# Kernel tuning notes

Measured on AMD Instinct MI355X. Metric: run time of the kernel, lower is better.

The kernel has to match this reference:

```python
import jax, jax.numpy as jnp
import numpy as np

P = 100   # num_proxies
N = 1024  # num_samples
D = 512


def _edge_index():
    # complete bipartite proxy<->sample graph, both directions, plus self-loops
    # (PyG GATConv adds self-loops for all nodes by default)
    p = np.arange(P)
    s = np.arange(P, P + N)
    src_ps = np.repeat(p, N)   # proxy -> sample
    dst_ps = np.tile(s, P)
    loops = np.arange(P + N)
    src = np.concatenate([src_ps, dst_ps, loops]).astype(np.int32)
    dst = np.concatenate([dst_ps, src_ps, loops]).astype(np.int32)
    return jnp.asarray(src), jnp.asarray(dst)


def setup_inputs() -> dict:
    key = jax.random.key(0)
    ks = jax.random.split(key, 10)
    sc = 1.0 / np.sqrt(D)
    src, dst = _edge_index()
    return {
        "x": jax.random.normal(ks[0], (N, D), jnp.float32),
        "proxies": jax.random.normal(ks[1], (P, D), jnp.float32),
        "W1": jax.random.normal(ks[2], (D, D), jnp.float32) * sc,
        "a_src1": jax.random.normal(ks[3], (D,), jnp.float32) * sc,
        "a_dst1": jax.random.normal(ks[4], (D,), jnp.float32) * sc,
        "b1": jnp.zeros((D,), jnp.float32),
        "W2": jax.random.normal(ks[5], (D, D), jnp.float32) * sc,
        "a_src2": jax.random.normal(ks[6], (D,), jnp.float32) * sc,
        "a_dst2": jax.random.normal(ks[7], (D,), jnp.float32) * sc,
        "b2": jnp.zeros((D,), jnp.float32),
        "fc_w": jax.random.normal(ks[8], (D, 100), jnp.float32) * sc,
        "fc_b": jnp.zeros((100,), jnp.float32),
        "src": src,
        "dst": dst,
    }


def _gat_conv(x, src, dst, W, a_src, a_dst, b, n_nodes):
    # PyG GATConv, heads=1, concat=True, negative_slope=0.2
    h = x @ W                      # [n, D]
    l_src = h @ a_src              # [n]
    l_dst = h @ a_dst              # [n]
    e = jax.nn.leaky_relu(l_src[src] + l_dst[dst], 0.2)   # [E]
    # segment softmax over edges sharing the same destination
    e = e - jax.ops.segment_max(e, dst, num_segments=n_nodes)[dst]
    ex = jnp.exp(e)
    denom = jax.ops.segment_sum(ex, dst, num_segments=n_nodes)[dst]
    alpha = ex / denom             # [E]
    out = jax.ops.segment_sum(alpha[:, None] * h[src], dst, num_segments=n_nodes)
    return out + b


def reference(x, proxies, W1, a_src1, a_dst1, b1, W2, a_src2, a_dst2, b2, fc_w, fc_b, src, dst):
    n = P + N
    h = jnp.concatenate([proxies, x], axis=0)          # [P+N, D]
    h = jax.nn.relu(_gat_conv(h, src, dst, W1, a_src1, a_dst1, b1, n))
    # Dropout -> identity (eval)
    h = jax.nn.relu(_gat_conv(h, src, dst, W2, a_src2, a_dst2, b2, n))
    preds = h @ fc_w + fc_b                            # [P+N, 100]
    return preds[P:], h[P:]
```

## Files before the change

### kernel.cpp

```cpp
#include <hip/hip_runtime.h>

#define PP 100
#define NS 1024
#define NN 1124
#define DD 512
#define CC 100
#define NTHR 256
#define GT  512

typedef _Float16 f16;
typedef _Float16 f16x8 __attribute__((ext_vector_type(8)));
typedef float    f32x4 __attribute__((ext_vector_type(4)));

__device__ __forceinline__ float lk(float v) { return v > 0.f ? v : 0.2f * v; }
__device__ __forceinline__ f16 hif(float v) { return (f16)v; }
__device__ __forceinline__ f16 lof(float v) { return (f16)(v - (float)((f16)v)); }

#define MFMA16(a, b, c) __builtin_amdgcn_mfma_f32_16x16x32_f16(a, b, c, 0, 0, 0)


__device__ __forceinline__ void mgemm_core(
    const f16* __restrict__ Ah, const f16* __restrict__ Al,
    const f16* __restrict__ Bth, const f16* __restrict__ Btl,
    int K, int row0, int col0, f16* __restrict__ lds, f32x4 acc[2])
{
  const int t = threadIdx.x;
  const int lane = t & 63, w = t >> 6;
  const int wr = w >> 1, wc = w & 1;
  const bool isA = t < 256;
  const int tt = t & 255;
  const int srow = tt >> 2, su = tt & 3;
  const int lw = srow * 40 + su * 8;
  const int sec0 = isA ? 0 : 5120, sec1 = isA ? 2560 : 7680;
  const f16* g0 = isA ? Ah : Bth;
  const f16* g1 = isA ? Al : Btl;
  const size_t goff = (size_t)((isA ? row0 : col0) + srow) * K + su * 8;
  const int fra = wr * 16 + (lane & 15);
  const int frb = wc * 32 + (lane & 15);
  const int fu  = (lane >> 4) * 8;
  f32x4 p0 = *(const f32x4*)(g0 + goff);
  f32x4 p1 = *(const f32x4*)(g1 + goff);
  *(f32x4*)(lds + sec0 + lw) = p0;
  *(f32x4*)(lds + sec1 + lw) = p1;
  if (K > 32) {
    p0 = *(const f32x4*)(g0 + goff + 32);
    p1 = *(const f32x4*)(g1 + goff + 32);
  }
  __syncthreads();
  int cur = 0;
  for (int kt = 32; kt <= K; kt += 32) {
    f16* rb = lds + cur * 10240;
    f16* wb = lds + (cur ^ 1) * 10240;
    f16x8 ah  = *(const f16x8*)(rb + fra * 40 + fu);
    f16x8 al  = *(const f16x8*)(rb + 2560 + fra * 40 + fu);
    f16x8 bh0 = *(const f16x8*)(rb + 5120 + frb * 40 + fu);
    f16x8 bl0 = *(const f16x8*)(rb + 7680 + frb * 40 + fu);
    f16x8 bh1 = *(const f16x8*)(rb + 5120 + (frb + 16) * 40 + fu);
    f16x8 bl1 = *(const f16x8*)(rb + 7680 + (frb + 16) * 40 + fu);
    if (kt < K) {
      *(f32x4*)(wb + sec0 + lw) = p0;
      *(f32x4*)(wb + sec1 + lw) = p1;
      if (kt + 32 < K) {
        p0 = *(const f32x4*)(g0 + goff + kt + 32);
        p1 = *(const f32x4*)(g1 + goff + kt + 32);
      }
    }
    acc[0] = MFMA16(ah, bh0, acc[0]);
    acc[0] = MFMA16(al, bh0, acc[0]);
    acc[0] = MFMA16(ah, bl0, acc[0]);
    acc[1] = MFMA16(ah, bh1, acc[1]);
    acc[1] = MFMA16(al, bh1, acc[1]);
    acc[1] = MFMA16(ah, bl1, acc[1]);
    __syncthreads();
    cur ^= 1;
  }
}

__device__ __forceinline__ void agg_core(
    const float* __restrict__ lsrc, int kvalid,
    const float* __restrict__ ldb, const float* __restrict__ lsb,
    const f16* __restrict__ Bth, const f16* __restrict__ Btl,
    int K, int row0, int col0, int rvalid,
    const float* __restrict__ selfv,
    f16* __restrict__ outh, f16* __restrict__ outl,
    f16* __restrict__ lds, float* __restrict__ fred)
{
  const int t = threadIdx.x, lane = t & 63, w = t >> 6;
  const int wr = w >> 1, wc = w & 1;
  float* zred = fred;
  float* res  = fred + 256;
  float* riz  = fred + 320;
  float sm = -1e30f;
  for (int k = t; k < kvalid; k += GT) sm = fmaxf(sm, lsrc[k]);
#pragma unroll
  for (int off = 1; off < 64; off <<= 1) sm = fmaxf(sm, __shfl_xor(sm, off));
  if (lane == 0) zred[w] = sm;
  __syncthreads();
  sm = fmaxf(fmaxf(fmaxf(zred[0], zred[1]), fmaxf(zred[2], zred[3])),
             fmaxf(fmaxf(zred[4], zred[5]), fmaxf(zred[6], zred[7])));
  __syncthreads();
  const bool isA = t < 256;
  const int tt = t & 255;
  const int srow = tt >> 2, su = tt & 3;
  const int lw = srow * 40 + su * 8;
  bool rok = false; float ldr = 0.f, mr = 0.f;
  if (isA && (row0 + srow) < rvalid) {
    rok = true;
    ldr = ldb[row0 + srow];
    mr  = lk(fmaxf(sm, lsb[row0 + srow]) + ldr);
  }
  const size_t boff = (size_t)(col0 + srow) * K + su * 8;
  const int fra = wr * 16 + (lane & 15);
  const int frb = wc * 32 + (lane & 15);
  const int fu  = (lane >> 4) * 8;
  f32x4 acc[2] = {};
  float zacc = 0.f;
  f32x4 p0, p1;
  if (isA) {
    p0 = *(const f32x4*)(lsrc + su * 8);
    p1 = *(const f32x4*)(lsrc + su * 8 + 4);
  } else {
    p0 = *(const f32x4*)(Bth + boff);
    p1 = *(const f32x4*)(Btl + boff);
  }
  auto stage = [&](f16* buf, int kbase) {
    if (isA) {
      f16x8 ae, al8;
#pragma unroll
      for (int j = 0; j < 8; ++j) {
        const int k = kbase + su * 8 + j;
        const float lv = (j < 4) ? p0[j] : p1[j - 4];
        float f = 0.f;
        if (rok && k < kvalid) f = __expf(lk(lv + ldr) - mr);
        zacc += f;
        ae[j] = hif(f); al8[j] = lof(f);
      }
      *(f16x8*)(buf + lw) = ae;
      *(f16x8*)(buf + 2560 + lw) = al8;
    } else {
      *(f32x4*)(buf + 5120 + lw) = p0;
      *(f32x4*)(buf + 7680 + lw) = p1;
    }
  };
  auto prefetch = [&](int k) {
    if (isA) {
      p0 = *(const f32x4*)(lsrc + k + su * 8);
      p1 = *(const f32x4*)(lsrc + k + su * 8 + 4);
    } else {
      p0 = *(const f32x4*)(Bth + boff + k);
      p1 = *(const f32x4*)(Btl + boff + k);
    }
  };
  stage(lds, 0);
  if (K > 32) prefetch(32);
  __syncthreads();
  int cur = 0;
  for (int kt = 32; kt <= K; kt += 32) {
    f16* rb = lds + cur * 10240;
    f16* wb = lds + (cur ^ 1) * 10240;
    f16x8 ah  = *(const f16x8*)(rb + fra * 40 + fu);
    f16x8 al  = *(const f16x8*)(rb + 2560 + fra * 40 + fu);
    f16x8 bh0 = *(const f16x8*)(rb + 5120 + frb * 40 + fu);
    f16x8 bl0 = *(const f16x8*)(rb + 7680 + frb * 40 + fu);
    f16x8 bh1 = *(const f16x8*)(rb + 5120 + (frb + 16) * 40 + fu);
    f16x8 bl1 = *(const f16x8*)(rb + 7680 + (frb + 16) * 40 + fu);
    if (kt < K) {
      stage(wb, kt);
      if (kt + 32 < K) prefetch(kt + 32);
    }
    acc[0] = MFMA16(ah, bh0, acc[0]);
    acc[0] = MFMA16(al, bh0, acc[0]);
    acc[0] = MFMA16(ah, bl0, acc[0]);
    acc[1] = MFMA16(ah, bh1, acc[1]);
    acc[1] = MFMA16(al, bh1, acc[1]);
    acc[1] = MFMA16(ah, bl1, acc[1]);
    __syncthreads();
    cur ^= 1;
  }
  if (t < 256) zred[t] = zacc;
  __syncthreads();
  if (t < 64) {
    float z = zred[t * 4] + zred[t * 4 + 1] + zred[t * 4 + 2] + zred[t * 4 + 3];
    float es = 0.f, iz = 0.f;
    if (row0 + t < rvalid) {
      const float l2 = ldb[row0 + t], s2 = lsb[row0 + t];
      const float m2 = lk(fmaxf(sm, s2) + l2);
      es = __expf(lk(s2 + l2) - m2);
      iz = 1.f / (z + es);
    }
    res[t] = es; riz[t] = iz;
  }
  __syncthreads();
#pragma unroll
  for (int q = 0; q < 4; ++q) {
    const int rl = wr * 16 + (lane >> 4) * 4 + q;
    const int gr = row0 + rl;
    if (gr >= rvalid) continue;
    const float es = res[rl], iz = riz[rl];
#pragma unroll
    for (int n = 0; n < 2; ++n) {
      const int c = col0 + wc * 32 + n * 16 + (lane & 15);
      const float v = (acc[n][q] + es * selfv[(size_t)gr * DD + c]) * iz;
      outh[(size_t)gr * DD + c] = hif(v);
      outl[(size_t)gr * DD + c] = lof(v);
    }
  }
}

__device__ __forceinline__ void cvt_tile(
    const float* __restrict__ in, int R, int Cin,
    f16* __restrict__ oh, f16* __restrict__ ol, int ldo,
    int ti, int tj)
{
  const int t = threadIdx.x;
  const int gj0 = tj * 64 + (t & 31) * 2;
  const int i8  = (t >> 5) * 8;
  const bool c0 = gj0 < Cin, c1 = (gj0 + 1) < Cin;
  f16x8 vh0, vl0, vh1, vl1;
#pragma unroll
  for (int e = 0; e < 8; ++e) {
    const int gi = ti * 64 + i8 + e;
    float a = 0.f, b = 0.f;
    if (gi < R) {
      if (c0 && c1) {
        const float2 v = *(const float2*)(in + (size_t)gi * Cin + gj0);
        a = v.x; b = v.y;
      } else if (c0) {
        a = in[(size_t)gi * Cin + gj0];
      }
    }
    vh0[e] = hif(a); vl0[e] = lof(a);
    vh1[e] = hif(b); vl1[e] = lof(b);
  }
  const size_t o0 = (size_t)gj0 * ldo + ti * 64 + i8;
  *(f16x8*)(oh + o0) = vh0;
  *(f16x8*)(ol + o0) = vl0;
  const size_t o1 = o0 + ldo;
  *(f16x8*)(oh + o1) = vh1;
  *(f16x8*)(ol + o1) = vl1;
}

__global__ __launch_bounds__(NTHR) void prep1_k(
    const float* __restrict__ W1, const float* __restrict__ W2,
    const float* __restrict__ as1, const float* __restrict__ ad1,
    const float* __restrict__ as2, const float* __restrict__ ad2,
    float* __restrict__ v1s, float* __restrict__ v1d,
    float* __restrict__ v2s, float* __restrict__ v2d,
    float* __restrict__ ls2, float* __restrict__ ld2,
    float* __restrict__ M1pf, float* __restrict__ zP)
{
  const int u = blockIdx.x;
  if (u < 256) {
    const int wid  = u * 4 + (threadIdx.x >> 6);
    const int lane = threadIdx.x & 63;
    const int r = wid & 511;
    const bool l1 = (wid < 512);
    const float* W = l1 ? W1 : W2;
    const float4* a4 = (const float4*)(l1 ? as1 : as2);
    const float4* b4 = (const float4*)(l1 ? ad1 : ad2);
    const float4* w4 = (const float4*)(W + (size_t)r * DD);
    float4 w0 = w4[lane], w1 = w4[lane + 64];
    float4 a0 = a4[lane], a1 = a4[lane + 64];
    float4 b0 = b4[lane], b1 = b4[lane + 64];
    float s1 = w0.x * a0.x + w0.y * a0.y + w0.z * a0.z + w0.w * a0.w
             + w1.x * a1.x + w1.y * a1.y + w1.z * a1.z + w1.w * a1.w;
    float s2 = w0.x * b0.x + w0.y * b0.y + w0.z * b0.z + w0.w * b0.w
             + w1.x * b1.x + w1.y * b1.y + w1.z * b1.z + w1.w * b1.w;
#pragma unroll
    for (int off = 32; off > 0; off >>= 1) {
      s1 += __shfl_down(s1, off);
      s2 += __shfl_down(s2, off);
    }
    if (lane == 0) {
      (l1 ? v1s : v2s)[r] = s1;
      (l1 ? v1d : v2d)[r] = s2;
    }
  } else if (u == 256) {
    for (int i = threadIdx.x; i < 1152; i += NTHR) { ls2[i] = 0.f; ld2[i] = 0.f; }
    if (threadIdx.x < 128) zP[threadIdx.x] = 0.f;
  } else {
    float4* p4 = (float4*)M1pf + (size_t)(u - 257) * 800;
#pragma unroll
    for (int p = 0; p < 4; ++p) {
      const int i = threadIdx.x + p * 256;
      if (i < 800) p4[i] = make_float4(0.f, 0.f, 0.f, 0.f);
    }
  }
}

__global__ __launch_bounds__(NTHR) void prep2_k(
    const float* __restrict__ x, const float* __restrict__ prox,
    const float* __restrict__ W1, const float* __restrict__ W2,
    const float* __restrict__ fcw,
    const float* __restrict__ v1s, const float* __restrict__ v1d,
    f16* xth, f16* xtl, f16* pth, f16* ptl,
    f16* W1th, f16* W1tl, f16* W2th, f16* W2tl, f16* fwth, f16* fwtl,
    float* __restrict__ ls1, float* __restrict__ ld1)
{
  const int b = blockIdx.x;
  if (b < 64) {
    cvt_tile(W1, 512, 512, W1th, W1tl, 512, b >> 3, b & 7);
  } else if (b < 128) {
    cvt_tile(W2, 512, 512, W2th, W2tl, 512, (b - 64) >> 3, (b - 64) & 7);
  } else if (b < 256) {
    cvt_tile(x, NS, 512, xth, xtl, NS, (b - 128) >> 3, (b - 128) & 7);
  } else if (b < 272) {
    cvt_tile(prox, PP, 512, pth, ptl, 128, (b - 256) >> 3, (b - 256) & 7);
  } else if (b < 288) {
    cvt_tile(fcw, 512, CC, fwth, fwtl, 512, (b - 272) >> 1, (b - 272) & 1);
  } else {
    const int r    = (b - 288) * 4 + (threadIdx.x >> 6);
    const int lane = threadIdx.x & 63;
    if (r >= NN) return;
    const float* row = (r < PP) ? prox + (size_t)r * DD
                                : x + (size_t)(r - PP) * DD;
    const float4* r4 = (const float4*)row;
    const float4* s4 = (const float4*)v1s;
    const float4* d4 = (const float4*)v1d;
    float4 v0 = r4[lane], v1 = r4[lane + 64];
    float4 a0 = s4[lane], a1 = s4[lane + 64];
    float4 b0 = d4[lane], b1 = d4[lane + 64];
    float s1 = v0.x * a0.x + v0.y * a0.y + v0.z * a0.z + v0.w * a0.w
             + v1.x * a1.x + v1.y * a1.y + v1.z * a1.z + v1.w * a1.w;
    float s2 = v0.x * b0.x + v0.y * b0.y + v0.z * b0.z + v0.w * b0.w
             + v1.x * b1.x + v1.y * b1.y + v1.z * b1.z + v1.w * b1.w;
#pragma unroll
    for (int off = 32; off > 0; off >>= 1) {
      s1 += __shfl_down(s1, off);
      s2 += __shfl_down(s2, off);
    }
    if (lane == 0) { ls1[r] = s1; ld1[r] = s2; }
  }
}

__global__ __launch_bounds__(GT) void agg1x_k(
    const float* __restrict__ ls1, const float* __restrict__ ld1,
    const f16* __restrict__ pth, const f16* __restrict__ ptl,
    const f16* __restrict__ xth, const f16* __restrict__ xtl,
    const float* __restrict__ x,
    float* __restrict__ M1pf, float* __restrict__ zP,
    f16* __restrict__ M1h, f16* __restrict__ M1l)
{
  __shared__ __align__(16) f16 lds[20480];
  __shared__ float fred[384];
  const int b = blockIdx.x;
  if (b < 128) {
    const int row0 = (b >> 3) * 64, col0 = (b & 7) * 64;
    agg_core(ls1, PP, ld1 + PP, ls1 + PP, pth, ptl, 128, row0, col0, NS,
             x, M1h + (size_t)PP * DD, M1l + (size_t)PP * DD, lds, fred);
    return;
  }
  const int t = threadIdx.x, lane = t & 63, w = t >> 6;
  const int wr = w >> 1, wc = w & 1;
  const int b2 = b - 128;
  const int tile = b2 >> 2, chunk = b2 & 3;
  const int row0 = (tile >> 3) * 64, col0 = (tile & 7) * 64;
  const int k0 = chunk * 256;
  const float* lsrc = ls1 + PP;
  float sm = -1e30f;
  for (int k = t; k < NS; k += GT) sm = fmaxf(sm, lsrc[k]);
#pragma unroll
  for (int off = 1; off < 64; off <<= 1) sm = fmaxf(sm, __shfl_xor(sm, off));
  if (lane == 0) fred[w] = sm;
  __syncthreads();
  sm = fmaxf(fmaxf(fmaxf(fred[0], fred[1]), fmaxf(fred[2], fred[3])),
             fmaxf(fmaxf(fred[4], fred[5]), fmaxf(fred[6], fred[7])));
  __syncthreads();
  const bool isA = t < 256;
  const int tt = t & 255;
  const int srow = tt >> 2, su = tt & 3;
  const int lw = srow * 40 + su * 8;
  bool rok = false; float ldr = 0.f, mr = 0.f;
  if (isA && (row0 + srow) < PP) {
    rok = true;
    ldr = ld1[row0 + srow];
    mr  = lk(fmaxf(sm, ls1[row0 + srow]) + ldr);
  }
  const size_t boff = (size_t)(col0 + srow) * NS + k0 + su * 8;
  const int fra = wr * 16 + (lane & 15);
  const int frb = wc * 32 + (lane & 15);
  const int fu  = (lane >> 4) * 8;
  f32x4 acc[2] = {};
  float zacc = 0.f;
  f32x4 p0, p1;
  auto prefetch = [&](int k) {
    if (isA) {
      p0 = *(const f32x4*)(lsrc + k0 + k + su * 8);
      p1 = *(const f32x4*)(lsrc + k0 + k + su * 8 + 4);
    } else {
      p0 = *(const f32x4*)(xth + boff + k);
      p1 = *(const f32x4*)(xtl + boff + k);
    }
  };
  auto stage = [&](f16* buf) {
    if (isA) {
      f16x8 ae, al8;
#pragma unroll
      for (int j = 0; j < 8; ++j) {
        const float lv = (j < 4) ? p0[j] : p1[j - 4];
        float f = 0.f;
        if (rok) f = __expf(lk(lv + ldr) - mr);
        zacc += f;
        ae[j] = hif(f); al8[j] = lof(f);
      }
      *(f16x8*)(buf + lw) = ae;
      *(f16x8*)(buf + 2560 + lw) = al8;
    } else {
      *(f32x4*)(buf + 5120 + lw) = p0;
      *(f32x4*)(buf + 7680 + lw) = p1;
    }
  };
  prefetch(0);
  stage(lds);
  prefetch(32);
  __syncthreads();
  int cur = 0;
  for (int kt = 32; kt <= 256; kt += 32) {
    f16* rb = lds + cur * 10240;
    f16* wb = lds + (cur ^ 1) * 10240;
    f16x8 ah  = *(const f16x8*)(rb + fra * 40 + fu);
    f16x8 al  = *(const f16x8*)(rb + 2560 + fra * 40 + fu);
    f16x8 bh0 = *(const f16x8*)(rb + 5120 + frb * 40 + fu);
    f16x8 bl0 = *(const f16x8*)(rb + 7680 + frb * 40 + fu);
    f16x8 bh1 = *(const f16x8*)(rb + 5120 + (frb + 16) * 40 + fu);
    f16x8 bl1 = *(const f16x8*)(rb + 7680 + (frb + 16) * 40 + fu);
    if (kt < 256) {
      stage(wb);
      if (kt + 32 < 256) prefetch(kt + 32);
    }
    acc[0] = MFMA16(ah, bh0, acc[0]);
    acc[0] = MFMA16(al, bh0, acc[0]);
    acc[0] = MFMA16(ah, bl0, acc[0]);
    acc[1] = MFMA16(ah, bh1, acc[1]);
    acc[1] = MFMA16(al, bh1, acc[1]);
    acc[1] = MFMA16(ah, bl1, acc[1]);
    __syncthreads();
    cur ^= 1;
  }
  if (col0 == 0) {
    if (t < 256) fred[t] = zacc;
    __syncthreads();
    if (t < 64) {
      const int r = row0 + t;
      if (r < PP) {
        float z = fred[t * 4] + fred[t * 4 + 1] + fred[t * 4 + 2] + fred[t * 4 + 3];
        atomicAdd(&zP[r], z);
      }
    }
  }
#pragma unroll
  for (int q = 0; q < 4; ++q) {
    const int gr = row0 + wr * 16 + (lane >> 4) * 4 + q;
    if (gr >= PP) continue;
#pragma unroll
    for (int n = 0; n < 2; ++n) {
      const int c = col0 + wc * 32 + n * 16 + (lane & 15);
      atomicAdd(&M1pf[(size_t)gr * DD + c], acc[n][q]);
    }
  }
}

__global__ __launch_bounds__(GT) void h1_k(
    const f16* __restrict__ M1h, const f16* __restrict__ M1l,
    const float* __restrict__ M1pf, const float* __restrict__ zP,
    const float* __restrict__ ls1, const float* __restrict__ ld1,
    const float* __restrict__ prox,
    const f16* __restrict__ W1th, const f16* __restrict__ W1tl,
    const float* __restrict__ b1,
    const float* __restrict__ v2s, const float* __restrict__ v2d,
    float* __restrict__ h1, f16* __restrict__ h1pth, f16* __restrict__ h1ptl,
    float* __restrict__ ls2, float* __restrict__ ld2)
{
  __shared__ __align__(16) f16 lds[20480];
  __shared__ float fred[384];
  float* esA = fred + 256;
  float* izA = fred + 320;
  const int t = threadIdx.x, lane = t & 63, w = t >> 6;
  const int wr = w >> 1, wc = w & 1;
  const int b = blockIdx.x;
  const int row0 = (b >> 3) * 64, col0 = (b & 7) * 64;
  const bool hasP = (row0 < 128);
  if (hasP) {
    float sm = -1e30f;
    for (int k = t; k < NS; k += GT) sm = fmaxf(sm, ls1[PP + k]);
#pragma unroll
    for (int off = 1; off < 64; off <<= 1) sm = fmaxf(sm, __shfl_xor(sm, off));
    if (lane == 0) fred[w] = sm;
    __syncthreads();
    sm = fmaxf(fmaxf(fmaxf(fred[0], fred[1]), fmaxf(fred[2], fred[3])),
               fmaxf(fmaxf(fred[4], fred[5]), fmaxf(fred[6], fred[7])));
    if (t < 64) {
      const int r = row0 + t;
      float es = 0.f, iz = 0.f;
      if (r < PP) {
        const float ldr = ld1[r];
        const float m = lk(fmaxf(sm, ls1[r]) + ldr);
        es = __expf(lk(ls1[r] + ldr) - m);
        iz = 1.f / (zP[r] + es);
      }
      esA[t] = es; izA[t] = iz;
    }
    __syncthreads();
  }
  const bool isA = t < 256;
  const int tt = t & 255;
  const int srow = tt >> 2, su = tt & 3;
  const int lw = srow * 40 + su * 8;
  const int ar = row0 + srow;
  const bool isP = isA && (ar < PP);
  const size_t aoff = (size_t)ar * DD + su * 8;
  const size_t boff = (size_t)(col0 + srow) * DD + su * 8;
  const int fra = wr * 16 + (lane & 15);
  const int frb = wc * 32 + (lane & 15);
  const int fu  = (lane >> 4) * 8;
  const float esr = isP ? esA[srow] : 0.f;
  const float izr = isP ? izA[srow] : 0.f;
  f32x4 qa0, qa1, qb0, qb1;
  auto loadS = [&](int k) {
    if (isA) {
      if (isP) {
        qa0 = *(const f32x4*)(M1pf + aoff + k);
        qa1 = *(const f32x4*)(M1pf + aoff + k + 4);
        qb0 = *(const f32x4*)(prox + aoff + k);
        qb1 = *(const f32x4*)(prox + aoff + k + 4);
      } else {
        qa0 = *(const f32x4*)(M1h + aoff + k);
        qa1 = *(const f32x4*)(M1l + aoff + k);
      }
    } else {
      qa0 = *(const f32x4*)(W1th + boff + k);
      qa1 = *(const f32x4*)(W1tl + boff + k);
    }
  };
  auto storeS = [&](f16* wb) {
    if (isA) {
      if (isP) {
        f16x8 hh, ll;
#pragma unroll
        for (int j = 0; j < 8; ++j) {
          const float pv = (j < 4) ? qa0[j] : qa1[j - 4];
          const float xv = (j < 4) ? qb0[j] : qb1[j - 4];
          const float v = (pv + esr * xv) * izr;
          hh[j] = hif(v); ll[j] = lof(v);
        }
        *(f16x8*)(wb + lw) = hh;
        *(f16x8*)(wb + 2560 + lw) = ll;
      } else {
        *(f32x4*)(wb + lw) = qa0;
        *(f32x4*)(wb + 2560 + lw) = qa1;
      }
    } else {
      *(f32x4*)(wb + 5120 + lw) = qa0;
      *(f32x4*)(wb + 7680 + lw) = qa1;
    }
  };
  f32x4 acc[2] = {};
  loadS(0);
  storeS(lds);
  loadS(32);
  __syncthreads();
  int cur = 0;
  for (int kt = 32; kt <= DD; kt += 32) {
    f16* rb = lds + cur * 10240;
    f16* wb = lds + (cur ^ 1) * 10240;
    f16x8 ah  = *(const f16x8*)(rb + fra * 40 + fu);
    f16x8 al  = *(const f16x8*)(rb + 2560 + fra * 40 + fu);
    f16x8 bh0 = *(const f16x8*)(rb + 5120 + frb * 40 + fu);
    f16x8 bl0 = *(const f16x8*)(rb + 7680 + frb * 40 + fu);
    f16x8 bh1 = *(const f16x8*)(rb + 5120 + (frb + 16) * 40 + fu);
    f16x8 bl1 = *(const f16x8*)(rb + 7680 + (frb + 16) * 40 + fu);
    if (kt < DD) {
      storeS(wb);
      if (kt + 32 < DD) loadS(kt + 32);
    }
    acc[0] = MFMA16(ah, bh0, acc[0]);
    acc[0] = MFMA16(al, bh0, acc[0]);
    acc[0] = MFMA16(ah, bl0, acc[0]);
    acc[1] = MFMA16(ah, bh1, acc[1]);
    acc[1] = MFMA16(al, bh1, acc[1]);
    acc[1] = MFMA16(ah, bl1, acc[1]);
    __syncthreads();
    cur ^= 1;
  }
  const int c0 = col0 + wc * 32 + (lane & 15);
  const int c1 = c0 + 16;
  const float vs0 = v2s[c0], vs1 = v2s[c1];
  const float vd0 = v2d[c0], vd1 = v2d[c1];
  const float bb0 = b1[c0],  bb1 = b1[c1];
#pragma unroll
  for (int q = 0; q < 4; ++q) {
    const int r = row0 + wr * 16 + (lane >> 4) * 4 + q;
    if (r >= NN) continue;
    float ps = 0.f, pd = 0.f;
#pragma unroll
    for (int n = 0; n < 2; ++n) {
      const int c = (n == 0) ? c0 : c1;
      const float v = fmaxf(acc[n][q] + (n == 0 ? bb0 : bb1), 0.f);
      h1[(size_t)r * DD + c] = v;
      ps += v * (n == 0 ? vs0 : vs1);
      pd += v * (n == 0 ? vd0 : vd1);
      if (r < 128) {
        const size_t o = (size_t)c * 128 + r;
        f16 hh = (f16)0.f, ll = (f16)0.f;
        if (r < PP) { hh = hif(v); ll = lof(v); }
        h1pth[o] = hh; h1ptl[o] = ll;
      }
    }
#pragma unroll
    for (int off = 1; off < 16; off <<= 1) {
      ps += __shfl_xor(ps, off);
      pd += __shfl_xor(pd, off);
    }
    if ((lane & 15) == 0) {
      atomicAdd(&ls2[r], ps);
      atomicAdd(&ld2[r], pd);
    }
  }
}

__global__ __launch_bounds__(GT) void agg2x_k(
    const float* __restrict__ ls2, const float* __restrict__ ld2,
    const f16* __restrict__ h1pth, const f16* __restrict__ h1ptl,
    const float* __restrict__ h1,
    f16* __restrict__ M2h, f16* __restrict__ M2l)
{
  __shared__ __align__(16) f16 lds[20480];
  __shared__ float fred[384];
  const int b = blockIdx.x;
  const int row0 = (b >> 3) * 64, col0 = (b & 7) * 64;
  agg_core(ls2, PP, ld2 + PP, ls2 + PP, h1pth, h1ptl, 128, row0, col0, NS,
           h1 + (size_t)PP * DD, M2h, M2l, lds, fred);
}

__global__ __launch_bounds__(GT) void h2_k(
    const f16* __restrict__ M2h, const f16* __restrict__ M2l,
    const f16* __restrict__ W2th, const f16* __restrict__ W2tl,
    const float* __restrict__ b2, float* __restrict__ h2s,
    f16* __restrict__ h2h, f16* __restrict__ h2l)
{
  __shared__ __align__(16) f16 lds[20480];
  f32x4 acc[2] = {};
  const int t = threadIdx.x, lane = t & 63, w = t >> 6;
  const int wr = w >> 1, wc = w & 1;
  const int b = blockIdx.x;
  const int row0 = (b >> 3) * 64, col0 = (b & 7) * 64;
  mgemm_core(M2h, M2l, W2th, W2tl, DD, row0, col0, lds, acc);
#pragma unroll
  for (int q = 0; q < 4; ++q) {
    const int r = row0 + wr * 16 + (lane >> 4) * 4 + q;
#pragma unroll
    for (int n = 0; n < 2; ++n) {
      const int c = col0 + wc * 32 + n * 16 + (lane & 15);
      const float v = fmaxf(acc[n][q] + b2[c], 0.f);
      const size_t o = (size_t)r * DD + c;
      h2s[o] = v;
      h2h[o] = hif(v); h2l[o] = lof(v);
    }
  }
}

__global__ __launch_bounds__(GT) void fc_k(
    const f16* __restrict__ h2h, const f16* __restrict__ h2l,
    const f16* __restrict__ fwth, const f16* __restrict__ fwtl,
    const float* __restrict__ fcb, float* __restrict__ out)
{
  __shared__ __align__(16) f16 lds[20480];
  f32x4 acc[2] = {};
  const int t = threadIdx.x, lane = t & 63, w = t >> 6;
  const int wr = w >> 1, wc = w & 1;
  const int b = blockIdx.x;
  const int row0 = (b >> 1) * 64, col0 = (b & 1) * 64;
  mgemm_core(h2h, h2l, fwth, fwtl, DD, row0, col0, lds, acc);
#pragma unroll
  for (int q = 0; q < 4; ++q) {
    const int r = row0 + wr * 16 + (lane >> 4) * 4 + q;
#pragma unroll
    for (int n = 0; n < 2; ++n) {
      const int c = col0 + wc * 32 + n * 16 + (lane & 15);
      if (c < CC) out[(size_t)r * CC + c] = acc[n][q] + fcb[c];
    }
  }
}

extern "C" void kernel_launch(void* const* d_in, const int* in_sizes, int n_in,
                              void* d_out, int out_size, void* d_ws, size_t ws_size,
                              hipStream_t stream)
{
  const float* x    = (const float*)d_in[0];
  const float* prox = (const float*)d_in[1];
  const float* W1   = (const float*)d_in[2];
  const float* as1  = (const float*)d_in[3];
  const float* ad1  = (const float*)d_in[4];
  const float* b1   = (const float*)d_in[5];
  const float* W2   = (const float*)d_in[6];
  const float* as2  = (const float*)d_in[7];
  const float* ad2  = (const float*)d_in[8];
  const float* b2   = (const float*)d_in[9];
  const float* fcw  = (const float*)d_in[10];
  const float* fcb  = (const float*)d_in[11];
  float* out = (float*)d_out;

  float* F = (float*)d_ws;
  float* h1   = F; F += (size_t)NN * DD;
  float* ls1  = F; F += 1152;
  float* ld1  = F; F += 1152;
  float* ls2  = F; F += 1152;
  float* ld2  = F; F += 1152;
  float* v1s  = F; F += DD;
  float* v1d  = F; F += DD;
  float* v2s  = F; F += DD;
  float* v2d  = F; F += DD;
  float* M1pf = F; F += (size_t)128 * DD;
  float* zP   = F; F += 128;
  f16* H = (f16*)F;
  f16* M1h  = H; H += (size_t)1152 * DD;
  f16* M1l  = H; H += (size_t)1152 * DD;
  f16* M2h  = H; H += (size_t)NS * DD;
  f16* M2l  = H; H += (size_t)NS * DD;
  f16* xth  = H; H += (size_t)DD * NS;
  f16* xtl  = H; H += (size_t)DD * NS;
  f16* pth  = H; H += (size_t)DD * 128;
  f16* ptl  = H; H += (size_t)DD * 128;
  f16* W1th = H; H += (size_t)DD * DD;
  f16* W1tl = H; H += (size_t)DD * DD;
  f16* W2th = H; H += (size_t)DD * DD;
  f16* W2tl = H; H += (size_t)DD * DD;
  f16* fwth = H; H += (size_t)128 * DD;
  f16* fwtl = H; H += (size_t)128 * DD;
  f16* h2h  = H; H += (size_t)NS * DD;
  f16* h2l  = H; H += (size_t)NS * DD;
  f16* h1pth = H; H += (size_t)DD * 128;
  f16* h1ptl = H; H += (size_t)DD * 128;
  float* h2s = out + (size_t)NS * CC;

  prep1_k<<<dim3(273), dim3(NTHR), 0, stream>>>(W1, W2, as1, ad1, as2, ad2,
                                                v1s, v1d, v2s, v2d, ls2, ld2,
                                                M1pf, zP);
  prep2_k<<<dim3(569), dim3(NTHR), 0, stream>>>(x, prox, W1, W2, fcw, v1s, v1d,
      xth, xtl, pth, ptl, W1th, W1tl, W2th, W2tl, fwth, fwtl, ls1, ld1);
  agg1x_k<<<dim3(192), dim3(GT), 0, stream>>>(ls1, ld1, pth, ptl, xth, xtl,
                                              x, M1pf, zP, M1h, M1l);
  h1_k<<<dim3(144), dim3(GT), 0, stream>>>(M1h, M1l, M1pf, zP, ls1, ld1, prox,
                                           W1th, W1tl, b1, v2s, v2d,
                                           h1, h1pth, h1ptl, ls2, ld2);
  agg2x_k<<<dim3(128), dim3(GT), 0, stream>>>(ls2, ld2, h1pth, h1ptl, h1,
                                              M2h, M2l);
  h2_k<<<dim3(128), dim3(GT), 0, stream>>>(M2h, M2l, W2th, W2tl, b2,
                                           h2s, h2h, h2l);
  fc_k<<<dim3(32), dim3(GT), 0, stream>>>(h2h, h2l, fwth, fwtl, fcb, out);
}
```

Baseline: 140.3 us.

## Widen GEMM K-tile to 128 and split h2 to f16 pairs inside fc kernel

All MFMA GEMM loops now stage 128-wide K tiles per double-buffer step instead of 32, with a padded row stride and more registers for prefetch. This cuts the number of loop iterations and barriers and gives each global load more bytes. LDS per block grows to about 136KB, which limits occupancy to one block per CU. Separately, h2_k no longer writes f16 hi/lo copies of h2; fc_k reads the fp32 h2 and splits it while staging, removing one intermediate round trip through global memory.

```diff
diff --git a/kernel.cpp b/kernel.cpp
--- a/kernel.cpp
+++ b/kernel.cpp
@@ -18,6 +18,11 @@
 
 #define MFMA16(a, b, c) __builtin_amdgcn_mfma_f32_16x16x32_f16(a, b, c, 0, 0, 0)
 
+#define LROW   136
+#define SEC_AL 8704
+#define SEC_BH 17408
+#define SEC_BL 26112
+#define BUFSZ  34816
 
 __device__ __forceinline__ void mgemm_core(
     const f16* __restrict__ Ah, const f16* __restrict__ Al,
@@ -30,47 +35,62 @@
   const bool isA = t < 256;
   const int tt = t & 255;
   const int srow = tt >> 2, su = tt & 3;
-  const int lw = srow * 40 + su * 8;
-  const int sec0 = isA ? 0 : 5120, sec1 = isA ? 2560 : 7680;
+  const int lw = srow * LROW + su * 32;
+  const int sec0 = isA ? 0 : SEC_BH, sec1 = isA ? SEC_AL : SEC_BL;
   const f16* g0 = isA ? Ah : Bth;
   const f16* g1 = isA ? Al : Btl;
-  const size_t goff = (size_t)((isA ? row0 : col0) + srow) * K + su * 8;
+  const size_t goff = (size_t)((isA ? row0 : col0) + srow) * K + su * 32;
   const int fra = wr * 16 + (lane & 15);
   const int frb = wc * 32 + (lane & 15);
   const int fu  = (lane >> 4) * 8;
-  f32x4 p0 = *(const f32x4*)(g0 + goff);
-  f32x4 p1 = *(const f32x4*)(g1 + goff);
-  *(f32x4*)(lds + sec0 + lw) = p0;
-  *(f32x4*)(lds + sec1 + lw) = p1;
-  if (K > 32) {
-    p0 = *(const f32x4*)(g0 + goff + 32);
-    p1 = *(const f32x4*)(g1 + goff + 32);
-  }
+  f32x4 p[8];
+  auto pf = [&](int k) {
+#pragma unroll
+    for (int i = 0; i < 4; ++i) {
+      p[i]     = *(const f32x4*)(g0 + goff + k + i * 8);
+      p[4 + i] = *(const f32x4*)(g1 + goff + k + i * 8);
+    }
+  };
+  auto st = [&](f16* buf) {
+#pragma unroll
+    for (int i = 0; i < 4; ++i) {
+      *(f32x4*)(buf + sec0 + lw + i * 8) = p[i];
+      *(f32x4*)(buf + sec1 + lw + i * 8) = p[4 + i];
+    }
+  };
+  pf(0); st(lds);
+  if (K > 128) pf(128);
   __syncthreads();
   int cur = 0;
-  for (int kt = 32; kt <= K; kt += 32) {
-    f16* rb = lds + cur * 10240;
-    f16* wb = lds + (cur ^ 1) * 10240;
-    f16x8 ah  = *(const f16x8*)(rb + fra * 40 + fu);
-    f16x8 al  = *(const f16x8*)(rb + 2560 + fra * 40 + fu);
-    f16x8 bh0 = *(const f16x8*)(rb + 5120 + frb * 40 + fu);
-    f16x8 bl0 = *(const f16x8*)(rb + 7680 + frb * 40 + fu);
-    f16x8 bh1 = *(const f16x8*)(rb + 5120 + (frb + 16) * 40 + fu);
-    f16x8 bl1 = *(const f16x8*)(rb + 7680 + (frb + 16) * 40 + fu);
+  for (int kt = 128; kt <= K; kt += 128) {
+    f16* rb = lds + cur * BUFSZ;
+    f16* wb = lds + (cur ^ 1) * BUFSZ;
+    f16x8 ah[4], al[4], bh0[4], bl0[4], bh1[4], bl1[4];
+#pragma unroll
+    for (int s = 0; s < 4; ++s) {
+      ah[s]  = *(const f16x8*)(rb + fra * LROW + s * 32 + fu);
+      al[s]  = *(const f16x8*)(rb + SEC_AL + fra * LROW + s * 32 + fu);
+      bh0[s] = *(const f16x8*)(rb + SEC_BH + frb * LROW + s * 32 + fu);
+      bl0[s] = *(const f16x8*)(rb + SEC_BL + frb * LROW + s * 32 + fu);
+      bh1[s] = *(const f16x8*)(rb + SEC_BH + (frb + 16) * LROW + s * 32 + fu);
+      bl1[s] = *(const f16x8*)(rb + SEC_BL + (frb + 16) * LROW + s * 32 + fu);
+    }
     if (kt < K) {
-      *(f32x4*)(wb + sec0 + lw) = p0;
-      *(f32x4*)(wb + sec1 + lw) = p1;
-      if (kt + 32 < K) {
-        p0 = *(const f32x4*)(g0 + goff + kt + 32);
-        p1 = *(const f32x4*)(g1 + goff + kt + 32);
-      }
-    }
-    acc[0] = MFMA16(ah, bh0, acc[0]);
-    acc[0] = MFMA16(al, bh0, acc[0]);
-    acc[0] = MFMA16(ah, bl0, acc[0]);
-    acc[1] = MFMA16(ah, bh1, acc[1]);
-    acc[1] = MFMA16(al, bh1, acc[1]);
-    acc[1] = MFMA16(ah, bl1, acc[1]);
+      st(wb);
+      if (kt + 128 < K) pf(kt + 128);
+    }
+#pragma unroll
+    for (int s = 0; s < 4; ++s) {
+      acc[0] = MFMA16(ah[s], bh0[s], acc[0]);
+      acc[0] = MFMA16(al[s], bh0[s], acc[0]);
+      acc[0] = MFMA16(ah[s], bl0[s], acc[0]);
+    }
+#pragma unroll
+    for (int s = 0; s < 4; ++s) {
+      acc[1] = MFMA16(ah[s], bh1[s], acc[1]);
+      acc[1] = MFMA16(al[s], bh1[s], acc[1]);
+      acc[1] = MFMA16(ah[s], bl1[s], acc[1]);
+    }
     __syncthreads();
     cur ^= 1;
   }
@@ -102,78 +122,95 @@
   const bool isA = t < 256;
   const int tt = t & 255;
   const int srow = tt >> 2, su = tt & 3;
-  const int lw = srow * 40 + su * 8;
+  const int lw = srow * LROW + su * 32;
   bool rok = false; float ldr = 0.f, mr = 0.f;
   if (isA && (row0 + srow) < rvalid) {
     rok = true;
     ldr = ldb[row0 + srow];
     mr  = lk(fmaxf(sm, lsb[row0 + srow]) + ldr);
   }
-  const size_t boff = (size_t)(col0 + srow) * K + su * 8;
+  const size_t boff = (size_t)(col0 + srow) * K + su * 32;
   const int fra = wr * 16 + (lane & 15);
   const int frb = wc * 32 + (lane & 15);
   const int fu  = (lane >> 4) * 8;
   f32x4 acc[2] = {};
   float zacc = 0.f;
-  f32x4 p0, p1;
-  if (isA) {
-    p0 = *(const f32x4*)(lsrc + su * 8);
-    p1 = *(const f32x4*)(lsrc + su * 8 + 4);
-  } else {
-    p0 = *(const f32x4*)(Bth + boff);
-    p1 = *(const f32x4*)(Btl + boff);
-  }
+  f32x4 p[8];
+  auto prefetch = [&](int k) {
+    if (isA) {
+#pragma unroll
+      for (int i = 0; i < 8; ++i)
+        p[i] = *(const f32x4*)(lsrc + k + su * 32 + i * 4);
+    } else {
+#pragma unroll
+      for (int i = 0; i < 4; ++i) {
+        p[i]     = *(const f32x4*)(Bth + boff + k + i * 8);
+        p[4 + i] = *(const f32x4*)(Btl + boff + k + i * 8);
+      }
+    }
+  };
   auto stage = [&](f16* buf, int kbase) {
     if (isA) {
-      f16x8 ae, al8;
-#pragma unroll
-      for (int j = 0; j < 8; ++j) {
-        const int k = kbase + su * 8 + j;
-        const float lv = (j < 4) ? p0[j] : p1[j - 4];
-        float f = 0.f;
-        if (rok && k < kvalid) f = __expf(lk(lv + ldr) - mr);
-        zacc += f;
-        ae[j] = hif(f); al8[j] = lof(f);
-      }
-      *(f16x8*)(buf + lw) = ae;
-      *(f16x8*)(buf + 2560 + lw) = al8;
+#pragma unroll
+      for (int g = 0; g < 2; ++g) {
+        f16x8 h0, h1v, l0, l1v;
+#pragma unroll
+        for (int j = 0; j < 16; ++j) {
+          const int k = kbase + su * 32 + g * 16 + j;
+          const float lv = p[g * 4 + (j >> 2)][j & 3];
+          float f = 0.f;
+          if (rok && k < kvalid) f = __expf(lk(lv + ldr) - mr);
+          zacc += f;
+          if (j < 8) { h0[j] = hif(f); l0[j] = lof(f); }
+          else       { h1v[j - 8] = hif(f); l1v[j - 8] = lof(f); }
+        }
+        *(f16x8*)(buf + lw + g * 16)              = h0;
+        *(f16x8*)(buf + lw + g * 16 + 8)          = h1v;
+        *(f16x8*)(buf + SEC_AL + lw + g * 16)     = l0;
+        *(f16x8*)(buf + SEC_AL + lw + g * 16 + 8) = l1v;
+      }
     } else {
-      *(f32x4*)(buf + 5120 + lw) = p0;
-      *(f32x4*)(buf + 7680 + lw) = p1;
+#pragma unroll
+      for (int i = 0; i < 4; ++i) {
+        *(f32x4*)(buf + SEC_BH + lw + i * 8) = p[i];
+        *(f32x4*)(buf + SEC_BL + lw + i * 8) = p[4 + i];
+      }
     }
   };
-  auto prefetch = [&](int k) {
-    if (isA) {
-      p0 = *(const f32x4*)(lsrc + k + su * 8);
-      p1 = *(const f32x4*)(lsrc + k + su * 8 + 4);
-    } else {
-      p0 = *(const f32x4*)(Bth + boff + k);
-      p1 = *(const f32x4*)(Btl + boff + k);
-    }
-  };
+  prefetch(0);
   stage(lds, 0);
-  if (K > 32) prefetch(32);
+  if (K > 128) prefetch(128);
   __syncthreads();
   int cur = 0;
-  for (int kt = 32; kt <= K; kt += 32) {
-    f16* rb = lds + cur * 10240;
-    f16* wb = lds + (cur ^ 1) * 10240;
-    f16x8 ah  = *(const f16x8*)(rb + fra * 40 + fu);
-    f16x8 al  = *(const f16x8*)(rb + 2560 + fra * 40 + fu);
-    f16x8 bh0 = *(const f16x8*)(rb + 5120 + frb * 40 + fu);
-    f16x8 bl0 = *(const f16x8*)(rb + 7680 + frb * 40 + fu);
-    f16x8 bh1 = *(const f16x8*)(rb + 5120 + (frb + 16) * 40 + fu);
-    f16x8 bl1 = *(const f16x8*)(rb + 7680 + (frb + 16) * 40 + fu);
+  for (int kt = 128; kt <= K; kt += 128) {
+    f16* rb = lds + cur * BUFSZ;
+    f16* wb = lds + (cur ^ 1) * BUFSZ;
+    f16x8 ah[4], al[4], bh0[4], bl0[4], bh1[4], bl1[4];
+#pragma unroll
+    for (int s = 0; s < 4; ++s) {
+      ah[s]  = *(const f16x8*)(rb + fra * LROW + s * 32 + fu);
+      al[s]  = *(const f16x8*)(rb + SEC_AL + fra * LROW + s * 32 + fu);
+      bh0[s] = *(const f16x8*)(rb + SEC_BH + frb * LROW + s * 32 + fu);
+      bl0[s] = *(const f16x8*)(rb + SEC_BL + frb * LROW + s * 32 + fu);
+      bh1[s] = *(const f16x8*)(rb + SEC_BH + (frb + 16) * LROW + s * 32 + fu);
+      bl1[s] = *(const f16x8*)(rb + SEC_BL + (frb + 16) * LROW + s * 32 + fu);
+    }
     if (kt < K) {
       stage(wb, kt);
-      if (kt + 32 < K) prefetch(kt + 32);
-    }
-    acc[0] = MFMA16(ah, bh0, acc[0]);
-    acc[0] = MFMA16(al, bh0, acc[0]);
-    acc[0] = MFMA16(ah, bl0, acc[0]);
-    acc[1] = MFMA16(ah, bh1, acc[1]);
-    acc[1] = MFMA16(al, bh1, acc[1]);
-    acc[1] = MFMA16(ah, bl1, acc[1]);
+      if (kt + 128 < K) prefetch(kt + 128);
+    }
+#pragma unroll
+    for (int s = 0; s < 4; ++s) {
+      acc[0] = MFMA16(ah[s], bh0[s], acc[0]);
+      acc[0] = MFMA16(al[s], bh0[s], acc[0]);
+      acc[0] = MFMA16(ah[s], bl0[s], acc[0]);
+    }
+#pragma unroll
+    for (int s = 0; s < 4; ++s) {
+      acc[1] = MFMA16(ah[s], bh1[s], acc[1]);
+      acc[1] = MFMA16(al[s], bh1[s], acc[1]);
+      acc[1] = MFMA16(ah[s], bl1[s], acc[1]);
+    }
     __syncthreads();
     cur ^= 1;
   }
@@ -341,7 +378,7 @@
     float* __restrict__ M1pf, float* __restrict__ zP,
     f16* __restrict__ M1h, f16* __restrict__ M1l)
 {
-  __shared__ __align__(16) f16 lds[20480];
+  __shared__ __align__(16) f16 lds[69632];
   __shared__ float fred[384];
   const int b = blockIdx.x;
   if (b < 128) {
@@ -369,71 +406,91 @@
   const bool isA = t < 256;
   const int tt = t & 255;
   const int srow = tt >> 2, su = tt & 3;
-  const int lw = srow * 40 + su * 8;
+  const int lw = srow * LROW + su * 32;
   bool rok = false; float ldr = 0.f, mr = 0.f;
   if (isA && (row0 + srow) < PP) {
     rok = true;
     ldr = ld1[row0 + srow];
     mr  = lk(fmaxf(sm, ls1[row0 + srow]) + ldr);
   }
-  const size_t boff = (size_t)(col0 + srow) * NS + k0 + su * 8;
+  const size_t boff = (size_t)(col0 + srow) * NS + k0 + su * 32;
   const int fra = wr * 16 + (lane & 15);
   const int frb = wc * 32 + (lane & 15);
   const int fu  = (lane >> 4) * 8;
   f32x4 acc[2] = {};
   float zacc = 0.f;
-  f32x4 p0, p1;
+  f32x4 p[8];
   auto prefetch = [&](int k) {
     if (isA) {
-      p0 = *(const f32x4*)(lsrc + k0 + k + su * 8);
-      p1 = *(const f32x4*)(lsrc + k0 + k + su * 8 + 4);
+#pragma unroll
+      for (int i = 0; i < 8; ++i)
+        p[i] = *(const f32x4*)(lsrc + k0 + k + su * 32 + i * 4);
     } else {
-      p0 = *(const f32x4*)(xth + boff + k);
-      p1 = *(const f32x4*)(xtl + boff + k);
+#pragma unroll
+      for (int i = 0; i < 4; ++i) {
+        p[i]     = *(const f32x4*)(xth + boff + k + i * 8);
+        p[4 + i] = *(const f32x4*)(xtl + boff + k + i * 8);
+      }
     }
   };
   auto stage = [&](f16* buf) {
     if (isA) {
-      f16x8 ae, al8;
-#pragma unroll
-      for (int j = 0; j < 8; ++j) {
-        const float lv = (j < 4) ? p0[j] : p1[j - 4];
-        float f = 0.f;
-        if (rok) f = __expf(lk(lv + ldr) - mr);
-        zacc += f;
-        ae[j] = hif(f); al8[j] = lof(f);
-      }
-      *(f16x8*)(buf + lw) = ae;
-      *(f16x8*)(buf + 2560 + lw) = al8;
+#pragma unroll
+      for (int g = 0; g < 2; ++g) {
+        f16x8 h0, h1v, l0, l1v;
+#pragma unroll
+        for (int j = 0; j < 16; ++j) {
+          const float lv = p[g * 4 + (j >> 2)][j & 3];
+          float f = 0.f;
+          if (rok) f = __expf(lk(lv + ldr) - mr);
+          zacc += f;
+          if (j < 8) { h0[j] = hif(f); l0[j] = lof(f); }
+          else       { h1v[j - 8] = hif(f); l1v[j - 8] = lof(f); }
+        }
+        *(f16x8*)(buf + lw + g * 16)              = h0;
+        *(f16x8*)(buf + lw + g * 16 + 8)          = h1v;
+        *(f16x8*)(buf + SEC_AL + lw + g * 16)     = l0;
+        *(f16x8*)(buf + SEC_AL + lw + g * 16 + 8) = l1v;
+      }
     } else {
-      *(f32x4*)(buf + 5120 + lw) = p0;
-      *(f32x4*)(buf + 7680 + lw) = p1;
+#pragma unroll
+      for (int i = 0; i < 4; ++i) {
+        *(f32x4*)(buf + SEC_BH + lw + i * 8) = p[i];
+        *(f32x4*)(buf + SEC_BL + lw + i * 8) = p[4 + i];
+      }
     }
   };
   prefetch(0);
   stage(lds);
-  prefetch(32);
+  prefetch(128);
   __syncthreads();
   int cur = 0;
-  for (int kt = 32; kt <= 256; kt += 32) {
-    f16* rb = lds + cur * 10240;
-    f16* wb = lds + (cur ^ 1) * 10240;
-    f16x8 ah  = *(const f16x8*)(rb + fra * 40 + fu);
-    f16x8 al  = *(const f16x8*)(rb + 2560 + fra * 40 + fu);
-    f16x8 bh0 = *(const f16x8*)(rb + 5120 + frb * 40 + fu);
-    f16x8 bl0 = *(const f16x8*)(rb + 7680 + frb * 40 + fu);
-    f16x8 bh1 = *(const f16x8*)(rb + 5120 + (frb + 16) * 40 + fu);
-    f16x8 bl1 = *(const f16x8*)(rb + 7680 + (frb + 16) * 40 + fu);
-    if (kt < 256) {
-      stage(wb);
-      if (kt + 32 < 256) prefetch(kt + 32);
-    }
-    acc[0] = MFMA16(ah, bh0, acc[0]);
-    acc[0] = MFMA16(al, bh0, acc[0]);
-    acc[0] = MFMA16(ah, bl0, acc[0]);
-    acc[1] = MFMA16(ah, bh1, acc[1]);
-    acc[1] = MFMA16(al, bh1, acc[1]);
-    acc[1] = MFMA16(ah, bl1, acc[1]);
+  for (int kt = 128; kt <= 256; kt += 128) {
+    f16* rb = lds + cur * BUFSZ;
+    f16* wb = lds + (cur ^ 1) * BUFSZ;
+    f16x8 ah[4], al[4], bh0[4], bl0[4], bh1[4], bl1[4];
+#pragma unroll
+    for (int s = 0; s < 4; ++s) {
+      ah[s]  = *(const f16x8*)(rb + fra * LROW + s * 32 + fu);
+      al[s]  = *(const f16x8*)(rb + SEC_AL + fra * LROW + s * 32 + fu);
+      bh0[s] = *(const f16x8*)(rb + SEC_BH + frb * LROW + s * 32 + fu);
+      bl0[s] = *(const f16x8*)(rb + SEC_BL + frb * LROW + s * 32 + fu);
+      bh1[s] = *(const f16x8*)(rb + SEC_BH + (frb + 16) * LROW + s * 32 + fu);
+      bl1[s] = *(const f16x8*)(rb + SEC_BL + (frb + 16) * LROW + s * 32 + fu);
+    }
+    if (kt < 256) stage(wb);
+#pragma unroll
+    for (int s = 0; s < 4; ++s) {
+      acc[0] = MFMA16(ah[s], bh0[s], acc[0]);
+      acc[0] = MFMA16(al[s], bh0[s], acc[0]);
+      acc[0] = MFMA16(ah[s], bl0[s], acc[0]);
+    }
+#pragma unroll
+    for (int s = 0; s < 4; ++s) {
+      acc[1] = MFMA16(ah[s], bh1[s], acc[1]);
+      acc[1] = MFMA16(al[s], bh1[s], acc[1]);
+      acc[1] = MFMA16(ah[s], bl1[s], acc[1]);
+    }
     __syncthreads();
     cur ^= 1;
   }
@@ -471,7 +528,7 @@
     float* __restrict__ h1, f16* __restrict__ h1pth, f16* __restrict__ h1ptl,
     float* __restrict__ ls2, float* __restrict__ ld2)
 {
-  __shared__ __align__(16) f16 lds[20480];
+  __shared__ __align__(16) f16 lds[69632];
   __shared__ float fred[384];
   float* esA = fred + 256;
   float* izA = fred + 320;
@@ -505,80 +562,109 @@
   const bool isA = t < 256;
   const int tt = t & 255;
   const int srow = tt >> 2, su = tt & 3;
-  const int lw = srow * 40 + su * 8;
+  const int lw = srow * LROW + su * 32;
   const int ar = row0 + srow;
   const bool isP = isA && (ar < PP);
-  const size_t aoff = (size_t)ar * DD + su * 8;
-  const size_t boff = (size_t)(col0 + srow) * DD + su * 8;
+  const size_t aoff = (size_t)ar * DD + su * 32;
+  const size_t boff = (size_t)(col0 + srow) * DD + su * 32;
   const int fra = wr * 16 + (lane & 15);
   const int frb = wc * 32 + (lane & 15);
   const int fu  = (lane >> 4) * 8;
   const float esr = isP ? esA[srow] : 0.f;
   const float izr = isP ? izA[srow] : 0.f;
-  f32x4 qa0, qa1, qb0, qb1;
+  f32x4 qa[8], qb[8];
   auto loadS = [&](int k) {
     if (isA) {
       if (isP) {
-        qa0 = *(const f32x4*)(M1pf + aoff + k);
-        qa1 = *(const f32x4*)(M1pf + aoff + k + 4);
-        qb0 = *(const f32x4*)(prox + aoff + k);
-        qb1 = *(const f32x4*)(prox + aoff + k + 4);
+#pragma unroll
+        for (int i = 0; i < 8; ++i) {
+          qa[i] = *(const f32x4*)(M1pf + aoff + k + i * 4);
+          qb[i] = *(const f32x4*)(prox + aoff + k + i * 4);
+        }
       } else {
-        qa0 = *(const f32x4*)(M1h + aoff + k);
-        qa1 = *(const f32x4*)(M1l + aoff + k);
+#pragma unroll
+        for (int i = 0; i < 4; ++i) {
+          qa[i]     = *(const f32x4*)(M1h + aoff + k + i * 8);
+          qa[4 + i] = *(const f32x4*)(M1l + aoff + k + i * 8);
+        }
       }
     } else {
-      qa0 = *(const f32x4*)(W1th + boff + k);
-      qa1 = *(const f32x4*)(W1tl + boff + k);
+#pragma unroll
+      for (int i = 0; i < 4; ++i) {
+        qa[i]     = *(const f32x4*)(W1th + boff + k + i * 8);
+        qa[4 + i] = *(const f32x4*)(W1tl + boff + k + i * 8);
+      }
     }
   };
   auto storeS = [&](f16* wb) {
     if (isA) {
       if (isP) {
-        f16x8 hh, ll;
-#pragma unroll
-        for (int j = 0; j < 8; ++j) {
-          const float pv = (j < 4) ? qa0[j] : qa1[j - 4];
-          const float xv = (j < 4) ? qb0[j] : qb1[j - 4];
-          const float v = (pv + esr * xv) * izr;
-          hh[j] = hif(v); ll[j] = lof(v);
+#pragma unroll
+        for (int g = 0; g < 2; ++g) {
+          f16x8 h0, h1v, l0, l1v;
+#pragma unroll
+          for (int j = 0; j < 16; ++j) {
+            const float pv = qa[g * 4 + (j >> 2)][j & 3];
+            const float xv = qb[g * 4 + (j >> 2)][j & 3];
+            const float v = (pv + esr * xv) * izr;
+            if (j < 8) { h0[j] = hif(v); l0[j] = lof(v); }
+            else       { h1v[j - 8] = hif(v); l1v[j - 8] = lof(v); }
+          }
+          *(f16x8*)(wb + lw + g * 16)              = h0;
+          *(f16x8*)(wb + lw + g * 16 + 8)          = h1v;
+          *(f16x8*)(wb + SEC_AL + lw + g * 16)     = l0;
+          *(f16x8*)(wb + SEC_AL + lw + g * 16 + 8) = l1v;
         }
-        *(f16x8*)(wb + lw) = hh;
-        *(f16x8*)(wb + 2560 + lw) = ll;
       } else {
-        *(f32x4*)(wb + lw) = qa0;
-        *(f32x4*)(wb + 2560 + lw) = qa1;
+#pragma unroll
+        for (int i = 0; i < 4; ++i) {
+          *(f32x4*)(wb + lw + i * 8)          = qa[i];
+          *(f32x4*)(wb + SEC_AL + lw + i * 8) = qa[4 + i];
+        }
       }
     } else {
-      *(f32x4*)(wb + 5120 + lw) = qa0;
-      *(f32x4*)(wb + 7680 + lw) = qa1;
+#pragma unroll
+      for (int i = 0; i < 4; ++i) {
+        *(f32x4*)(wb + SEC_BH + lw + i * 8) = qa[i];
+        *(f32x4*)(wb + SEC_BL + lw + i * 8) = qa[4 + i];
+      }
     }
   };
   f32x4 acc[2] = {};
   loadS(0);
   storeS(lds);
-  loadS(32);
+  loadS(128);
   __syncthreads();
   int cur = 0;
-  for (int kt = 32; kt <= DD; kt += 32) {
-    f16* rb = lds + cur * 10240;
-    f16* wb = lds + (cur ^ 1) * 10240;
-    f16x8 ah  = *(const f16x8*)(rb + fra * 40 + fu);
-    f16x8 al  = *(const f16x8*)(rb + 2560 + fra * 40 + fu);
-    f16x8 bh0 = *(const f16x8*)(rb + 5120 + frb * 40 + fu);
-    f16x8 bl0 = *(const f16x8*)(rb + 7680 + frb * 40 + fu);
-    f16x8 bh1 = *(const f16x8*)(rb + 5120 + (frb + 16) * 40 + fu);
-    f16x8 bl1 = *(const f16x8*)(rb + 7680 + (frb + 16) * 40 + fu);
+  for (int kt = 128; kt <= DD; kt += 128) {
+    f16* rb = lds + cur * BUFSZ;
+    f16* wb = lds + (cur ^ 1) * BUFSZ;
+    f16x8 ah[4], al[4], bh0[4], bl0[4], bh1[4], bl1[4];
+#pragma unroll
+    for (int s = 0; s < 4; ++s) {
+      ah[s]  = *(const f16x8*)(rb + fra * LROW + s * 32 + fu);
+      al[s]  = *(const f16x8*)(rb + SEC_AL + fra * LROW + s * 32 + fu);
+      bh0[s] = *(const f16x8*)(rb + SEC_BH + frb * LROW + s * 32 + fu);
+      bl0[s] = *(const f16x8*)(rb + SEC_BL + frb * LROW + s * 32 + fu);
+      bh1[s] = *(const f16x8*)(rb + SEC_BH + (frb + 16) * LROW + s * 32 + fu);
+      bl1[s] = *(const f16x8*)(rb + SEC_BL + (frb + 16) * LROW + s * 32 + fu);
+    }
     if (kt < DD) {
       storeS(wb);
-      if (kt + 32 < DD) loadS(kt + 32);
-    }
-    acc[0] = MFMA16(ah, bh0, acc[0]);
-    acc[0] = MFMA16(al, bh0, acc[0]);
-    acc[0] = MFMA16(ah, bl0, acc[0]);
-    acc[1] = MFMA16(ah, bh1, acc[1]);
-    acc[1] = MFMA16(al, bh1, acc[1]);
-    acc[1] = MFMA16(ah, bl1, acc[1]);
+      if (kt + 128 < DD) loadS(kt + 128);
+    }
+#pragma unroll
+    for (int s = 0; s < 4; ++s) {
+      acc[0] = MFMA16(ah[s], bh0[s], acc[0]);
+      acc[0] = MFMA16(al[s], bh0[s], acc[0]);
+      acc[0] = MFMA16(ah[s], bl0[s], acc[0]);
+    }
+#pragma unroll
+    for (int s = 0; s < 4; ++s) {
+      acc[1] = MFMA16(ah[s], bh1[s], acc[1]);
+      acc[1] = MFMA16(al[s], bh1[s], acc[1]);
+      acc[1] = MFMA16(ah[s], bl1[s], acc[1]);
+    }
     __syncthreads();
     cur ^= 1;
   }
@@ -624,7 +710,7 @@
     const float* __restrict__ h1,
     f16* __restrict__ M2h, f16* __restrict__ M2l)
 {
-  __shared__ __align__(16) f16 lds[20480];
+  __shared__ __align__(16) f16 lds[69632];
   __shared__ float fred[384];
   const int b = blockIdx.x;
   const int row0 = (b >> 3) * 64, col0 = (b & 7) * 64;
@@ -635,10 +721,9 @@
 __global__ __launch_bounds__(GT) void h2_k(
     const f16* __restrict__ M2h, const f16* __restrict__ M2l,
     const f16* __restrict__ W2th, const f16* __restrict__ W2tl,
-    const float* __restrict__ b2, float* __restrict__ h2s,
-    f16* __restrict__ h2h, f16* __restrict__ h2l)
-{
-  __shared__ __align__(16) f16 lds[20480];
+    const float* __restrict__ b2, float* __restrict__ h2s)
+{
+  __shared__ __align__(16) f16 lds[69632];
   f32x4 acc[2] = {};
   const int t = threadIdx.x, lane = t & 63, w = t >> 6;
   const int wr = w >> 1, wc = w & 1;
@@ -652,25 +737,106 @@
     for (int n = 0; n < 2; ++n) {
       const int c = col0 + wc * 32 + n * 16 + (lane & 15);
       const float v = fmaxf(acc[n][q] + b2[c], 0.f);
-      const size_t o = (size_t)r * DD + c;
-      h2s[o] = v;
-      h2h[o] = hif(v); h2l[o] = lof(v);
+      h2s[(size_t)r * DD + c] = v;
     }
   }
 }
 
 __global__ __launch_bounds__(GT) void fc_k(
-    const f16* __restrict__ h2h, const f16* __restrict__ h2l,
+    const float* __restrict__ h2s,
     const f16* __restrict__ fwth, const f16* __restrict__ fwtl,
     const float* __restrict__ fcb, float* __restrict__ out)
 {
-  __shared__ __align__(16) f16 lds[20480];
+  __shared__ __align__(16) f16 lds[69632];
   f32x4 acc[2] = {};
   const int t = threadIdx.x, lane = t & 63, w = t >> 6;
   const int wr = w >> 1, wc = w & 1;
   const int b = blockIdx.x;
   const int row0 = (b >> 1) * 64, col0 = (b & 1) * 64;
-  mgemm_core(h2h, h2l, fwth, fwtl, DD, row0, col0, lds, acc);
+  const bool isA = t < 256;
+  const int tt = t & 255;
+  const int srow = tt >> 2, su = tt & 3;
+  const int lw = srow * LROW + su * 32;
+  const size_t aoff = (size_t)(row0 + srow) * DD + su * 32;
+  const size_t boff = (size_t)(col0 + srow) * DD + su * 32;
+  const int fra = wr * 16 + (lane & 15);
+  const int frb = wc * 32 + (lane & 15);
+  const int fu  = (lane >> 4) * 8;
+  f32x4 qa[8];
+  auto loadS = [&](int k) {
+    if (isA) {
+#pragma unroll
+      for (int i = 0; i < 8; ++i)
+        qa[i] = *(const f32x4*)(h2s + aoff + k + i * 4);
+    } else {
+#pragma unroll
+      for (int i = 0; i < 4; ++i) {
+        qa[i]     = *(const f32x4*)(fwth + boff + k + i * 8);
+        qa[4 + i] = *(const f32x4*)(fwtl + boff + k + i * 8);
+      }
+    }
+  };
+  auto storeS = [&](f16* wb) {
+    if (isA) {
+#pragma unroll
+      for (int g = 0; g < 2; ++g) {
+        f16x8 h0, h1v, l0, l1v;
+#pragma unroll
+        for (int j = 0; j < 16; ++j) {
+          const float v = qa[g * 4 + (j >> 2)][j & 3];
+          if (j < 8) { h0[j] = hif(v); l0[j] = lof(v); }
+          else       { h1v[j - 8] = hif(v); l1v[j - 8] = lof(v); }
+        }
+        *(f16x8*)(wb + lw + g * 16)              = h0;
+        *(f16x8*)(wb + lw + g * 16 + 8)          = h1v;
+        *(f16x8*)(wb + SEC_AL + lw + g * 16)     = l0;
+        *(f16x8*)(wb + SEC_AL + lw + g * 16 + 8) = l1v;
+      }
+    } else {
+#pragma unroll
+      for (int i = 0; i < 4; ++i) {
+        *(f32x4*)(wb + SEC_BH + lw + i * 8) = qa[i];
+        *(f32x4*)(wb + SEC_BL + lw + i * 8) = qa[4 + i];
+      }
+    }
+  };
+  loadS(0);
+  storeS(lds);
+  loadS(128);
+  __syncthreads();
+  int cur = 0;
+  for (int kt = 128; kt <= DD; kt += 128) {
+    f16* rb = lds + cur * BUFSZ;
+    f16* wb = lds + (cur ^ 1) * BUFSZ;
+    f16x8 ah[4], al[4], bh0[4], bl0[4], bh1[4], bl1[4];
+#pragma unroll
+    for (int s = 0; s < 4; ++s) {
+      ah[s]  = *(const f16x8*)(rb + fra * LROW + s * 32 + fu);
+      al[s]  = *(const f16x8*)(rb + SEC_AL + fra * LROW + s * 32 + fu);
+      bh0[s] = *(const f16x8*)(rb + SEC_BH + frb * LROW + s * 32 + fu);
+      bl0[s] = *(const f16x8*)(rb + SEC_BL + frb * LROW + s * 32 + fu);
+      bh1[s] = *(const f16x8*)(rb + SEC_BH + (frb + 16) * LROW + s * 32 + fu);
+      bl1[s] = *(const f16x8*)(rb + SEC_BL + (frb + 16) * LROW + s * 32 + fu);
+    }
+    if (kt < DD) {
+      storeS(wb);
+      if (kt + 128 < DD) loadS(kt + 128);
+    }
+#pragma unroll
+    for (int s = 0; s < 4; ++s) {
+      acc[0] = MFMA16(ah[s], bh0[s], acc[0]);
+      acc[0] = MFMA16(al[s], bh0[s], acc[0]);
+      acc[0] = MFMA16(ah[s], bl0[s], acc[0]);
+    }
+#pragma unroll
+    for (int s = 0; s < 4; ++s) {
+      acc[1] = MFMA16(ah[s], bh1[s], acc[1]);
+      acc[1] = MFMA16(al[s], bh1[s], acc[1]);
+      acc[1] = MFMA16(ah[s], bl1[s], acc[1]);
+    }
+    __syncthreads();
+    cur ^= 1;
+  }
 #pragma unroll
   for (int q = 0; q < 4; ++q) {
     const int r = row0 + wr * 16 + (lane >> 4) * 4 + q;
@@ -727,8 +893,6 @@
   f16* W2tl = H; H += (size_t)DD * DD;
   f16* fwth = H; H += (size_t)128 * DD;
   f16* fwtl = H; H += (size_t)128 * DD;
-  f16* h2h  = H; H += (size_t)NS * DD;
-  f16* h2l  = H; H += (size_t)NS * DD;
   f16* h1pth = H; H += (size_t)DD * 128;
   f16* h1ptl = H; H += (size_t)DD * 128;
   float* h2s = out + (size_t)NS * CC;
@@ -745,7 +909,6 @@
                                            h1, h1pth, h1ptl, ls2, ld2);
   agg2x_k<<<dim3(128), dim3(GT), 0, stream>>>(ls2, ld2, h1pth, h1ptl, h1,
                                               M2h, M2l);
-  h2_k<<<dim3(128), dim3(GT), 0, stream>>>(M2h, M2l, W2th, W2tl, b2,
-                                           h2s, h2h, h2l);
-  fc_k<<<dim3(32), dim3(GT), 0, stream>>>(h2h, h2l, fwth, fwtl, fcb, out);
-}
+  h2_k<<<dim3(128), dim3(GT), 0, stream>>>(M2h, M2l, W2th, W2tl, b2, h2s);
+  fc_k<<<dim3(32), dim3(GT), 0, stream>>>(h2s, fwth, fwtl, fcb, out);
+}
```

Result: slower. 147.2 us (+4.9%).
